# Optimization experiments

Measured on AMD Instinct MI355X. Metric: run time of the kernel, lower is better.

Reference implementation:

```python
import jax, jax.numpy as jnp
import numpy as np

NEG_SLOPE = 0.2  # PyG GATConv default


def gat_conv(h, src, dst, n_nodes, W, a_src, a_dst, bias, concat):
    """PyG-style GATConv (single linear shared across src/dst, self-loops
    already included in src/dst). W: [heads*out, in]; a_*: [heads, out]."""
    heads, out = a_src.shape
    g = (h @ W.T).reshape(-1, heads, out)  # [N, H, D]
    # per-node attention logits, then gather scalars per edge (PyG order)
    al_src = jnp.einsum('nhd,hd->nh', g, a_src)  # [N, H]
    al_dst = jnp.einsum('nhd,hd->nh', g, a_dst)
    e = jax.nn.leaky_relu(al_src[src] + al_dst[dst], NEG_SLOPE)  # [E, H]
    # segment softmax over incoming edges of each dst node
    e_max = jax.ops.segment_max(e, dst, num_segments=n_nodes)
    e_exp = jnp.exp(e - e_max[dst])
    denom = jax.ops.segment_sum(e_exp, dst, num_segments=n_nodes)
    alpha = e_exp / denom[dst]  # every node has a self-loop -> denom > 0
    msg = g[src] * alpha[..., None]  # [E, H, D]
    out_n = jax.ops.segment_sum(msg, dst, num_segments=n_nodes)  # [N, H, D]
    if concat:
        out_n = out_n.reshape(n_nodes, heads * out)
    else:
        out_n = out_n.mean(axis=1)
    return out_n + bias


def setup_inputs() -> dict:
    key = jax.random.key(0)
    ks = jax.random.split(key, 20)
    N, M = 100000, 1600000
    node_dim, edge_dim, global_dim = 12, 5, 11
    hidden, heads, num_targets = 32, 4, 4
    in1 = node_dim + global_dim  # 23
    s = 0.1
    inp = {
        'x': jax.random.normal(ks[0], (N, node_dim), jnp.float32),
        'edge_index': jax.random.randint(ks[1], (2, M), 0, N, jnp.int32),
        'edge_attr': jax.random.normal(ks[2], (M, edge_dim), jnp.float32),
        'u': jax.random.normal(ks[3], (1, global_dim), jnp.float32),
        # conv1: in1 -> hidden per head, concat
        'W1': jax.random.normal(ks[4], (heads * hidden, in1), jnp.float32) * s,
        'a_src1': jax.random.normal(ks[5], (heads, hidden), jnp.float32) * s,
        'a_dst1': jax.random.normal(ks[6], (heads, hidden), jnp.float32) * s,
        'b1': jnp.zeros((heads * hidden,), jnp.float32),
        # conv2: heads*hidden -> hidden, mean over heads
        'W2': jax.random.normal(ks[7], (heads * hidden, heads * hidden), jnp.float32) * s,
        'a_src2': jax.random.normal(ks[8], (heads, hidden), jnp.float32) * s,
        'a_dst2': jax.random.normal(ks[9], (heads, hidden), jnp.float32) * s,
        'b2': jnp.zeros((hidden,), jnp.float32),
        # decoder: (2*hidden + edge_dim) -> 2*hidden -> hidden -> num_targets
        'dw1': jax.random.normal(ks[10], (2 * hidden, 2 * hidden + edge_dim), jnp.float32) * s,
        'db1': jnp.zeros((2 * hidden,), jnp.float32),
        'dw2': jax.random.normal(ks[11], (hidden, 2 * hidden), jnp.float32) * s,
        'db2': jnp.zeros((hidden,), jnp.float32),
        'dw3': jax.random.normal(ks[12], (num_targets, hidden), jnp.float32) * s,
        'db3': jnp.zeros((num_targets,), jnp.float32),
    }
    return inp


def reference(x, edge_index, edge_attr, u, W1, a_src1, a_dst1, b1,
              W2, a_src2, a_dst2, b2, dw1, db1, dw2, db2, dw3, db3):
    N = x.shape[0]
    loop = jnp.arange(N, dtype=edge_index.dtype)
    src = jnp.concatenate([edge_index[0], loop])  # add self-loops (PyG default)
    dst = jnp.concatenate([edge_index[1], loop])

    u_node = jnp.broadcast_to(u, (N, u.shape[-1]))
    h = jnp.concatenate([x, u_node], axis=-1)  # [N, 23]

    h = jax.nn.elu(gat_conv(h, src, dst, N, W1, a_src1, a_dst1, b1, True))
    h = jax.nn.elu(gat_conv(h, src, dst, N, W2, a_src2, a_dst2, b2, False))

    s0, d0 = edge_index[0], edge_index[1]
    e_in = jnp.concatenate([h[s0], h[d0], edge_attr], axis=-1)  # [M, 69]
    z = jax.nn.relu(e_in @ dw1.T + db1)
    z = jax.nn.relu(z @ dw2.T + db2)
    return z @ dw3.T + db3  # [M, num_targets]
```

## Files before the change

### kernel.cpp

```cpp
#include <hip/hip_runtime.h>

#define DEVINL __device__ __forceinline__

DEVINL float leakyf(float v) { return v > 0.f ? v : 0.2f * v; }
DEVINL float eluf(float v)   { return v > 0.f ? v : __expf(v) - 1.f; }

__global__ void __launch_bounds__(256) k_izero(int* __restrict__ p, int total) {
  int t = blockIdx.x * blockDim.x + threadIdx.x;
  if (t < total) p[t] = 0;
}

__global__ void __launch_bounds__(256) k_count(const int* __restrict__ ei,
                                               int* __restrict__ cnt, int M, int E) {
  int e = blockIdx.x * blockDim.x + threadIdx.x;
  if (e >= E) return;
  int d = (e < M) ? ei[M + e] : e - M;
  atomicAdd(&cnt[d], 1);
}

__global__ void __launch_bounds__(256) k_scan1(const int* __restrict__ cnt,
                                               int* __restrict__ off,
                                               int* __restrict__ bsum, int N) {
  __shared__ int sh[256];
  int i = blockIdx.x * 256 + threadIdx.x;
  int v = (i < N) ? cnt[i] : 0;
  sh[threadIdx.x] = v;
  __syncthreads();
  for (int o = 1; o < 256; o <<= 1) {
    int t = (threadIdx.x >= o) ? sh[threadIdx.x - o] : 0;
    __syncthreads();
    sh[threadIdx.x] += t;
    __syncthreads();
  }
  if (i < N) off[i] = sh[threadIdx.x] - v;
  if (threadIdx.x == 255) bsum[blockIdx.x] = sh[255];
}

__global__ void __launch_bounds__(512) k_scan2(int* __restrict__ bsum, int nb) {
  __shared__ int sh[512];
  int t = threadIdx.x;
  int v = (t < nb) ? bsum[t] : 0;
  sh[t] = v;
  __syncthreads();
  for (int o = 1; o < 512; o <<= 1) {
    int x = (t >= o) ? sh[t - o] : 0;
    __syncthreads();
    sh[t] += x;
    __syncthreads();
  }
  if (t < nb) bsum[t] = sh[t] - v;
}

__global__ void __launch_bounds__(256) k_scan3(int* __restrict__ off,
                                               const int* __restrict__ bsum,
                                               int* __restrict__ cur, int N, int E) {
  int i = blockIdx.x * 256 + threadIdx.x;
  if (i < N) { off[i] += bsum[i >> 8]; cur[i] = 0; }
  if (i == N) off[N] = E;
}

__global__ void __launch_bounds__(256) k_fill(const int* __restrict__ ei,
                                              const int* __restrict__ off,
                                              int* __restrict__ cur,
                                              int* __restrict__ ssrc,
                                              int* __restrict__ idst,
                                              int* __restrict__ ieid, int M, int E) {
  int e = blockIdx.x * blockDim.x + threadIdx.x;
  if (e >= E) return;
  int s, d, id;
  if (e < M) { s = ei[e]; d = ei[M + e]; id = e; }
  else       { s = e - M; d = s; id = -1; }
  int pos = off[d] + atomicAdd(&cur[d], 1);
  ssrc[pos] = s;
  idst[pos] = d;
  ieid[pos] = id;
}

__global__ void k_prep(const float* __restrict__ W1, const float* __restrict__ as1,
                       const float* __restrict__ ad1,
                       const float* __restrict__ W2, const float* __restrict__ as2,
                       const float* __restrict__ ad2,
                       float* __restrict__ wa1s, float* __restrict__ wa1d,
                       float* __restrict__ wa2s, float* __restrict__ wa2d) {
  int t = threadIdx.x;
  if (t < 92) {
    int h = t / 23, c = t % 23;
    float s1 = 0.f, s2 = 0.f;
    for (int dd = 0; dd < 32; ++dd) {
      float w = W1[(h * 32 + dd) * 23 + c];
      s1 += w * as1[h * 32 + dd];
      s2 += w * ad1[h * 32 + dd];
    }
    wa1s[t] = s1;
    wa1d[t] = s2;
  }
  {
    int h = t >> 7, c = t & 127;
    float s1 = 0.f, s2 = 0.f;
    for (int dd = 0; dd < 32; ++dd) {
      float w = W2[(h * 32 + dd) * 128 + c];
      s1 += w * as2[h * 32 + dd];
      s2 += w * ad2[h * 32 + dd];
    }
    wa2s[t] = s1;
    wa2d[t] = s2;
  }
}

__global__ void __launch_bounds__(128) k_g1(
    const float* __restrict__ x, const float* __restrict__ u,
    const float* __restrict__ W1,
    const float* __restrict__ wa1s, const float* __restrict__ wa1d,
    float* __restrict__ g1, float* __restrict__ al1s, float* __restrict__ al1d) {
  int n = blockIdx.x, k = threadIdx.x;
  __shared__ float hs[23];
  if (k < 12) hs[k] = x[n * 12 + k];
  else if (k < 23) hs[k] = u[k - 12];
  __syncthreads();
  const float* w = W1 + k * 23;
  float s = 0.f;
#pragma unroll
  for (int c = 0; c < 23; ++c) s += hs[c] * w[c];
  g1[n * 128 + k] = s;
  if (k < 8) {
    int h = k & 3;
    const float* wa = (k < 4 ? wa1s : wa1d) + h * 23;
    float t = 0.f;
#pragma unroll
    for (int c = 0; c < 23; ++c) t += hs[c] * wa[c];
    (k < 4 ? al1s : al1d)[n * 4 + h] = t;
  }
}

template <int MODE>
__global__ void __launch_bounds__(128) k_gat(
    const float* __restrict__ g, const float* __restrict__ als,
    const float* __restrict__ ald, const int* __restrict__ off,
    const int* __restrict__ ssrc, const float* __restrict__ bias,
    float* __restrict__ outp) {
  int d = blockIdx.x, t = threadIdx.x, h = t >> 5;
  float av = ald[d * 4 + h];
  int p0 = off[d], p1 = off[d + 1];
  float acc = 0.f, den = 0.f;
  int p = p0;
  for (; p + 4 <= p1; p += 4) {
    int s0 = ssrc[p], s1 = ssrc[p + 1], s2 = ssrc[p + 2], s3 = ssrc[p + 3];
    float l0 = als[s0 * 4 + h], l1 = als[s1 * 4 + h];
    float l2 = als[s2 * 4 + h], l3 = als[s3 * 4 + h];
    float g0 = g[(size_t)s0 * 128 + t], g1v = g[(size_t)s1 * 128 + t];
    float g2v = g[(size_t)s2 * 128 + t], g3v = g[(size_t)s3 * 128 + t];
    float w0 = __expf(leakyf(l0 + av)), w1 = __expf(leakyf(l1 + av));
    float w2 = __expf(leakyf(l2 + av)), w3 = __expf(leakyf(l3 + av));
    acc += w0 * g0 + w1 * g1v + w2 * g2v + w3 * g3v;
    den += (w0 + w1) + (w2 + w3);
  }
  for (; p < p1; ++p) {
    int s = ssrc[p];
    float w = __expf(leakyf(als[s * 4 + h] + av));
    acc += w * g[(size_t)s * 128 + t];
    den += w;
  }
  float v = acc / den;
  if (MODE == 0) {
    outp[(size_t)d * 128 + t] = eluf(v + bias[t]);
  } else {
    __shared__ float sh[128];
    sh[t] = v;
    __syncthreads();
    if (t < 32) {
      float m = 0.25f * (sh[t] + sh[t + 32] + sh[t + 64] + sh[t + 96]);
      outp[(size_t)d * 32 + t] = eluf(m + bias[t]);
    }
  }
}

__global__ void __launch_bounds__(128) k_g2t(
    const float* __restrict__ h2, const float* __restrict__ W2,
    const float* __restrict__ wa2s, const float* __restrict__ wa2d,
    float* __restrict__ g2, float* __restrict__ al2s, float* __restrict__ al2d,
    int N, int ntiles) {
  __shared__ float4 w4s[128][32];
  __shared__ float4 hs4[32][32];
  int t = threadIdx.x;

  for (int i = t; i < 4096; i += 128) {
    int c = i >> 5, kk = i & 31;
    float4 v = *(const float4*)(W2 + c * 128 + kk * 4);
    w4s[c][kk ^ ((c >> 2) & 31)] = v;
  }

  int m = t & 31, grp = t >> 5;
  int c0 = 4 * m;

  for (int tile = blockIdx.x; tile < ntiles; tile += gridDim.x) {
    int n0 = tile * 32;
    __syncthreads();
    for (int i = t; i < 1024; i += 128) {
      int n = i >> 5, kk = i & 31;
      int nn = n0 + n;
      hs4[n][kk] = (nn < N) ? *(const float4*)(h2 + (size_t)nn * 128 + kk * 4)
                            : make_float4(0.f, 0.f, 0.f, 0.f);
    }
    __syncthreads();

    float acc[8][4];
#pragma unroll
    for (int n = 0; n < 8; ++n)
#pragma unroll
      for (int j = 0; j < 4; ++j) acc[n][j] = 0.f;

#pragma unroll 8
    for (int kk = 0; kk < 32; ++kk) {
      float4 wj[4];
#pragma unroll
      for (int j = 0; j < 4; ++j) wj[j] = w4s[c0 + j][kk ^ m];
#pragma unroll
      for (int n = 0; n < 8; ++n) {
        float4 hv = hs4[grp * 8 + n][kk];
#pragma unroll
        for (int j = 0; j < 4; ++j) {
          acc[n][j] += hv.x * wj[j].x + hv.y * wj[j].y +
                       hv.z * wj[j].z + hv.w * wj[j].w;
        }
      }
    }
#pragma unroll
    for (int n = 0; n < 8; ++n) {
      int nn = n0 + grp * 8 + n;
      if (nn < N)
        *(float4*)(g2 + (size_t)nn * 128 + c0) =
            make_float4(acc[n][0], acc[n][1], acc[n][2], acc[n][3]);
    }

    for (int v = 0; v < 2; ++v) {
      int idx = t + 128 * v;
      int n = idx >> 3, j = idx & 7, h = j & 3;
      int nn = n0 + n;
      if (nn < N) {
        const float4* wa = (const float4*)((j < 4 ? wa2s : wa2d) + h * 128);
        float s = 0.f;
#pragma unroll
        for (int kk = 0; kk < 32; ++kk) {
          float4 a = hs4[n][kk];
          float4 w = wa[kk];
          s += a.x * w.x + a.y * w.y + a.z * w.z + a.w * w.w;
        }
        (j < 4 ? al2s : al2d)[(size_t)nn * 4 + h] = s;
      }
    }
  }
}

__global__ void __launch_bounds__(256) k_pq(
    const float* __restrict__ h3, const float* __restrict__ dw1,
    float* __restrict__ pq, int N) {
  __shared__ float4 ws4[64][16];
  __shared__ float ht[64][32];
  int t = threadIdx.x;
  for (int i = t; i < 4096; i += 256) {
    int k = i >> 6, c = i & 63;
    ((float*)&ws4[k][(c >> 2) ^ (k & 15)])[c & 3] = dw1[k * 69 + c];
  }
  int n0 = blockIdx.x * 64;
  for (int i = t; i < 2048; i += 256) {
    int n = i >> 5, c = i & 31;
    int nn = n0 + n;
    ht[n][c] = (nn < N) ? h3[(size_t)nn * 32 + c] : 0.f;
  }
  __syncthreads();
  int k2 = t & 127, sub = t >> 7;
  int k = k2 & 63, base4 = (k2 < 64) ? 0 : 8;
  float4 wr[8];
#pragma unroll
  for (int i = 0; i < 8; ++i) wr[i] = ws4[k][(base4 + i) ^ (k & 15)];
  for (int ii = 0; ii < 32; ++ii) {
    int n = sub * 32 + ii;
    const float4* hr = (const float4*)ht[n];
    float s = 0.f;
#pragma unroll
    for (int i = 0; i < 8; ++i) {
      float4 a = hr[i], w = wr[i];
      s += a.x * w.x + a.y * w.y + a.z * w.z + a.w * w.w;
    }
    int nn = n0 + n;
    if (nn < N) pq[(size_t)nn * 128 + k2] = s;
  }
}

__global__ void __launch_bounds__(256) k_dec(
    const float* __restrict__ pq, const int* __restrict__ ssrc,
    const int* __restrict__ idst, const int* __restrict__ ieid,
    const float* __restrict__ ea,
    const float* __restrict__ dw1, const float* __restrict__ db1,
    const float* __restrict__ dw2, const float* __restrict__ db2,
    const float* __restrict__ dw3, const float* __restrict__ db3,
    float* __restrict__ out, int E) {
  __shared__ float cs[64][8];
  __shared__ float w2s[32 * 64];
  __shared__ float w3s[4 * 32];
  __shared__ float bbs[104];
  int t = threadIdx.x;
  for (int i = t; i < 512; i += 256) {
    int k = i >> 3, c = i & 7;
    cs[k][c] = (c < 5) ? dw1[k * 69 + 64 + c] : 0.f;
  }
  for (int i = t; i < 2048; i += 256) w2s[i] = dw2[i];
  if (t < 128) w3s[t] = dw3[t];
  if (t < 64) bbs[t] = db1[t];
  else if (t < 96) bbs[t] = db2[t - 64];
  else if (t < 100) bbs[t] = db3[t - 96];
  __syncthreads();

  int pos = blockIdx.x * 256 + t;
  if (pos >= E) return;
  int eid = ieid[pos];
  if (eid < 0) return;
  int s = ssrc[pos], d = idst[pos];
  const float4* Pp = (const float4*)(pq + (size_t)s * 128);
  const float4* Qp = (const float4*)(pq + (size_t)d * 128 + 64);
  const float* ep = ea + (size_t)eid * 5;
  float e0 = ep[0], e1 = ep[1], e2 = ep[2], e3 = ep[3], e4 = ep[4];

  float z1[64];
#pragma unroll
  for (int i = 0; i < 16; ++i) {
    float4 p = Pp[i], q = Qp[i];
    z1[4 * i + 0] = p.x + q.x;
    z1[4 * i + 1] = p.y + q.y;
    z1[4 * i + 2] = p.z + q.z;
    z1[4 * i + 3] = p.w + q.w;
  }
#pragma unroll
  for (int k = 0; k < 64; ++k) {
    float acc = z1[k] + bbs[k];
    acc += cs[k][0] * e0 + cs[k][1] * e1 + cs[k][2] * e2 + cs[k][3] * e3 +
           cs[k][4] * e4;
    z1[k] = fmaxf(acc, 0.f);
  }

  float z2[32];
#pragma unroll
  for (int k = 0; k < 32; ++k) z2[k] = bbs[64 + k];
#pragma unroll
  for (int cq = 0; cq < 16; ++cq) {
    float4 e = make_float4(z1[cq * 4], z1[cq * 4 + 1], z1[cq * 4 + 2],
                           z1[cq * 4 + 3]);
#pragma unroll
    for (int k = 0; k < 32; ++k) {
      float4 w = *(const float4*)(w2s + k * 64 + cq * 4);
      z2[k] += e.x * w.x + e.y * w.y + e.z * w.z + e.w * w.w;
    }
  }
#pragma unroll
  for (int k = 0; k < 32; ++k) z2[k] = fmaxf(z2[k], 0.f);

  float o0 = bbs[96], o1 = bbs[97], o2 = bbs[98], o3 = bbs[99];
#pragma unroll
  for (int cq = 0; cq < 8; ++cq) {
    float4 e = make_float4(z2[cq * 4], z2[cq * 4 + 1], z2[cq * 4 + 2],
                           z2[cq * 4 + 3]);
    float4 wa = *(const float4*)(w3s + 0 * 32 + cq * 4);
    float4 wb = *(const float4*)(w3s + 1 * 32 + cq * 4);
    float4 wc = *(const float4*)(w3s + 2 * 32 + cq * 4);
    float4 wd = *(const float4*)(w3s + 3 * 32 + cq * 4);
    o0 += e.x * wa.x + e.y * wa.y + e.z * wa.z + e.w * wa.w;
    o1 += e.x * wb.x + e.y * wb.y + e.z * wb.z + e.w * wb.w;
    o2 += e.x * wc.x + e.y * wc.y + e.z * wc.z + e.w * wc.w;
    o3 += e.x * wd.x + e.y * wd.y + e.z * wd.z + e.w * wd.w;
  }
  *(float4*)(out + (size_t)eid * 4) = make_float4(o0, o1, o2, o3);
}

extern "C" void kernel_launch(void* const* d_in, const int* in_sizes, int n_in,
                              void* d_out, int out_size, void* d_ws, size_t ws_size,
                              hipStream_t stream) {
  const float* x   = (const float*)d_in[0];
  const int*   ei  = (const int*)d_in[1];
  const float* ea  = (const float*)d_in[2];
  const float* u   = (const float*)d_in[3];
  const float* W1  = (const float*)d_in[4];
  const float* as1 = (const float*)d_in[5];
  const float* ad1 = (const float*)d_in[6];
  const float* b1  = (const float*)d_in[7];
  const float* W2  = (const float*)d_in[8];
  const float* as2 = (const float*)d_in[9];
  const float* ad2 = (const float*)d_in[10];
  const float* b2  = (const float*)d_in[11];
  const float* dw1 = (const float*)d_in[12];
  const float* db1 = (const float*)d_in[13];
  const float* dw2 = (const float*)d_in[14];
  const float* db2 = (const float*)d_in[15];
  const float* dw3 = (const float*)d_in[16];
  const float* db3 = (const float*)d_in[17];
  float* out = (float*)d_out;

  const int N = in_sizes[0] / 12;
  const int M = in_sizes[1] / 2;
  const int E = M + N;

  float* ws = (float*)d_ws;
  float* A    = ws;
  float* B    = A + (size_t)N * 128;
  float* H3   = B;
  float* AL1S = B + (size_t)N * 128;
  float* AL1D = AL1S + (size_t)N * 4;
  float* AL2S = AL1D + (size_t)N * 4;
  float* AL2D = AL2S + (size_t)N * 4;
  float* WA1S = AL2D + (size_t)N * 4;
  float* WA1D = WA1S + 96;
  float* WA2S = WA1D + 96;
  float* WA2D = WA2S + 512;
  int* IOFF = (int*)(WA2D + 512);
  int* ICUR = IOFF + (N + 1);
  int* IBS  = ICUR + N;
  int* ISRC = IBS + 512;
  int* IDST = ISRC + E;
  int* IEID = IDST + E;

  int nb = (N + 255) / 256;
  int gE = (E + 255) / 256;

  k_izero<<<nb, 256, 0, stream>>>(ICUR, N);
  k_count<<<gE, 256, 0, stream>>>(ei, ICUR, M, E);
  k_scan1<<<nb, 256, 0, stream>>>(ICUR, IOFF, IBS, N);
  k_scan2<<<1, 512, 0, stream>>>(IBS, nb);
  k_scan3<<<(N + 256) / 256, 256, 0, stream>>>(IOFF, IBS, ICUR, N, E);
  k_fill<<<gE, 256, 0, stream>>>(ei, IOFF, ICUR, ISRC, IDST, IEID, M, E);

  k_prep<<<1, 512, 0, stream>>>(W1, as1, ad1, W2, as2, ad2, WA1S, WA1D, WA2S, WA2D);

  k_g1<<<N, 128, 0, stream>>>(x, u, W1, WA1S, WA1D, A, AL1S, AL1D);
  k_gat<0><<<N, 128, 0, stream>>>(A, AL1S, AL1D, IOFF, ISRC, b1, B);

  int ntiles = (N + 31) / 32;
  k_g2t<<<512, 128, 0, stream>>>(B, W2, WA2S, WA2D, A, AL2S, AL2D, N, ntiles);
  k_gat<1><<<N, 128, 0, stream>>>(A, AL2S, AL2D, IOFF, ISRC, b2, H3);

  k_pq<<<(N + 63) / 64, 256, 0, stream>>>(H3, dw1, A, N);
  k_dec<<<gE, 256, 0, stream>>>(A, ISRC, IDST, IEID, ea, dw1, db1, dw2, db2,
                                dw3, db3, out, E);
}
```

Baseline: 1.122 ms.

## Map one wavefront per node in GAT and process two edges per thread in decoder

The GAT aggregation kernels now assign one 64-lane wavefront per destination node. Each lane handles two features through float2 loads, and four nodes share each 256-thread block. The head-mean reduction uses shuffles in place of shared memory and a block barrier. The edge decoder now has each thread process two edges, so every weight read from LDS is reused across both edges, and the weights are stored as float4. This targets per-block overhead, LDS traffic and barriers, at the cost of higher register pressure in the decoder (two 32-float accumulators plus the inputs).

```diff
diff --git a/kernel.cpp b/kernel.cpp
--- a/kernel.cpp
+++ b/kernel.cpp
@@ -133,43 +133,59 @@
 }
 
 template <int MODE>
-__global__ void __launch_bounds__(128) k_gat(
+__global__ void __launch_bounds__(256) k_gat(
     const float* __restrict__ g, const float* __restrict__ als,
     const float* __restrict__ ald, const int* __restrict__ off,
     const int* __restrict__ ssrc, const float* __restrict__ bias,
-    float* __restrict__ outp) {
-  int d = blockIdx.x, t = threadIdx.x, h = t >> 5;
+    float* __restrict__ outp, int N) {
+  int wid = threadIdx.x >> 6, lane = threadIdx.x & 63;
+  int d = blockIdx.x * 4 + wid;
+  if (d >= N) return;
+  int h = lane >> 4;
   float av = ald[d * 4 + h];
   int p0 = off[d], p1 = off[d + 1];
-  float acc = 0.f, den = 0.f;
+  float accx = 0.f, accy = 0.f, den = 0.f;
   int p = p0;
   for (; p + 4 <= p1; p += 4) {
     int s0 = ssrc[p], s1 = ssrc[p + 1], s2 = ssrc[p + 2], s3 = ssrc[p + 3];
     float l0 = als[s0 * 4 + h], l1 = als[s1 * 4 + h];
     float l2 = als[s2 * 4 + h], l3 = als[s3 * 4 + h];
-    float g0 = g[(size_t)s0 * 128 + t], g1v = g[(size_t)s1 * 128 + t];
-    float g2v = g[(size_t)s2 * 128 + t], g3v = g[(size_t)s3 * 128 + t];
+    float2 G0 = *(const float2*)(g + (size_t)s0 * 128 + 2 * lane);
+    float2 G1 = *(const float2*)(g + (size_t)s1 * 128 + 2 * lane);
+    float2 G2 = *(const float2*)(g + (size_t)s2 * 128 + 2 * lane);
+    float2 G3 = *(const float2*)(g + (size_t)s3 * 128 + 2 * lane);
     float w0 = __expf(leakyf(l0 + av)), w1 = __expf(leakyf(l1 + av));
     float w2 = __expf(leakyf(l2 + av)), w3 = __expf(leakyf(l3 + av));
-    acc += w0 * g0 + w1 * g1v + w2 * g2v + w3 * g3v;
+    accx += w0 * G0.x + w1 * G1.x + w2 * G2.x + w3 * G3.x;
+    accy += w0 * G0.y + w1 * G1.y + w2 * G2.y + w3 * G3.y;
     den += (w0 + w1) + (w2 + w3);
   }
   for (; p < p1; ++p) {
     int s = ssrc[p];
     float w = __expf(leakyf(als[s * 4 + h] + av));
-    acc += w * g[(size_t)s * 128 + t];
+    float2 G = *(const float2*)(g + (size_t)s * 128 + 2 * lane);
+    accx += w * G.x;
+    accy += w * G.y;
     den += w;
   }
-  float v = acc / den;
+  float inv = 1.f / den;
+  float vx = accx * inv, vy = accy * inv;
   if (MODE == 0) {
-    outp[(size_t)d * 128 + t] = eluf(v + bias[t]);
+    float2 b = *(const float2*)(bias + 2 * lane);
+    float2 o;
+    o.x = eluf(vx + b.x);
+    o.y = eluf(vy + b.y);
+    *(float2*)(outp + (size_t)d * 128 + 2 * lane) = o;
   } else {
-    __shared__ float sh[128];
-    sh[t] = v;
-    __syncthreads();
-    if (t < 32) {
-      float m = 0.25f * (sh[t] + sh[t + 32] + sh[t + 64] + sh[t + 96]);
-      outp[(size_t)d * 32 + t] = eluf(m + bias[t]);
+    float sx = vx + __shfl_xor(vx, 16);
+    sx += __shfl_xor(sx, 32);
+    float sy = vy + __shfl_xor(vy, 16);
+    sy += __shfl_xor(sy, 32);
+    if (lane < 16) {
+      float2 o;
+      o.x = eluf(0.25f * sx + bias[2 * lane]);
+      o.y = eluf(0.25f * sy + bias[2 * lane + 1]);
+      *(float2*)(outp + (size_t)d * 32 + 2 * lane) = o;
     }
   }
 }
@@ -295,80 +311,120 @@
     const float* __restrict__ dw2, const float* __restrict__ db2,
     const float* __restrict__ dw3, const float* __restrict__ db3,
     float* __restrict__ out, int E) {
-  __shared__ float cs[64][8];
-  __shared__ float w2s[32 * 64];
-  __shared__ float w3s[4 * 32];
-  __shared__ float bbs[104];
+  __shared__ float4 w2s4[32][16];
+  __shared__ float4 ct4[5][16];
+  __shared__ float4 b1q[16];
+  __shared__ float4 b2q[8];
+  __shared__ float4 w3s4[4][8];
+  __shared__ float  db3s[4];
   int t = threadIdx.x;
   for (int i = t; i < 512; i += 256) {
-    int k = i >> 3, c = i & 7;
-    cs[k][c] = (c < 5) ? dw1[k * 69 + 64 + c] : 0.f;
-  }
-  for (int i = t; i < 2048; i += 256) w2s[i] = dw2[i];
-  if (t < 128) w3s[t] = dw3[t];
-  if (t < 64) bbs[t] = db1[t];
-  else if (t < 96) bbs[t] = db2[t - 64];
-  else if (t < 100) bbs[t] = db3[t - 96];
+    int k = i >> 4, cq = i & 15;
+    w2s4[k][cq] = *(const float4*)(dw2 + k * 64 + cq * 4);
+  }
+  if (t < 80) {
+    int c = t / 16, cq = t % 16;
+    float4 v;
+    v.x = dw1[(4 * cq + 0) * 69 + 64 + c];
+    v.y = dw1[(4 * cq + 1) * 69 + 64 + c];
+    v.z = dw1[(4 * cq + 2) * 69 + 64 + c];
+    v.w = dw1[(4 * cq + 3) * 69 + 64 + c];
+    ct4[c][cq] = v;
+  } else if (t < 96) {
+    b1q[t - 80] = *(const float4*)(db1 + 4 * (t - 80));
+  } else if (t < 104) {
+    b2q[t - 96] = *(const float4*)(db2 + 4 * (t - 96));
+  } else if (t < 136) {
+    int o = (t - 104) >> 3, cq = (t - 104) & 7;
+    w3s4[o][cq] = *(const float4*)(dw3 + o * 32 + 4 * cq);
+  } else if (t < 140) {
+    db3s[t - 136] = db3[t - 136];
+  }
   __syncthreads();
 
-  int pos = blockIdx.x * 256 + t;
-  if (pos >= E) return;
-  int eid = ieid[pos];
-  if (eid < 0) return;
-  int s = ssrc[pos], d = idst[pos];
-  const float4* Pp = (const float4*)(pq + (size_t)s * 128);
-  const float4* Qp = (const float4*)(pq + (size_t)d * 128 + 64);
-  const float* ep = ea + (size_t)eid * 5;
-  float e0 = ep[0], e1 = ep[1], e2 = ep[2], e3 = ep[3], e4 = ep[4];
-
-  float z1[64];
-#pragma unroll
-  for (int i = 0; i < 16; ++i) {
-    float4 p = Pp[i], q = Qp[i];
-    z1[4 * i + 0] = p.x + q.x;
-    z1[4 * i + 1] = p.y + q.y;
-    z1[4 * i + 2] = p.z + q.z;
-    z1[4 * i + 3] = p.w + q.w;
-  }
-#pragma unroll
-  for (int k = 0; k < 64; ++k) {
-    float acc = z1[k] + bbs[k];
-    acc += cs[k][0] * e0 + cs[k][1] * e1 + cs[k][2] * e2 + cs[k][3] * e3 +
-           cs[k][4] * e4;
-    z1[k] = fmaxf(acc, 0.f);
-  }
-
-  float z2[32];
-#pragma unroll
-  for (int k = 0; k < 32; ++k) z2[k] = bbs[64 + k];
-#pragma unroll
+  int pos0 = blockIdx.x * 512 + t;
+  int pos1 = pos0 + 256;
+  bool okA = pos0 < E, okB = pos1 < E;
+  int pa = okA ? pos0 : 0, pb = okB ? pos1 : 0;
+  int eA_ = okA ? ieid[pa] : -1;
+  int eB_ = okB ? ieid[pb] : -1;
+  bool wA = eA_ >= 0, wB = eB_ >= 0;
+  int eidA = wA ? eA_ : 0, eidB = wB ? eB_ : 0;
+  int sA = ssrc[pa], dA = idst[pa];
+  int sB = ssrc[pb], dB = idst[pb];
+  const float4* PA = (const float4*)(pq + (size_t)sA * 128);
+  const float4* QA = (const float4*)(pq + (size_t)dA * 128 + 64);
+  const float4* PB = (const float4*)(pq + (size_t)sB * 128);
+  const float4* QB = (const float4*)(pq + (size_t)dB * 128 + 64);
+  const float* eap = ea + (size_t)eidA * 5;
+  const float* ebp = ea + (size_t)eidB * 5;
+  float eAv[5], eBv[5];
+#pragma unroll
+  for (int c = 0; c < 5; ++c) { eAv[c] = eap[c]; eBv[c] = ebp[c]; }
+
+  float z2a[32], z2b[32];
+#pragma unroll
+  for (int kq = 0; kq < 8; ++kq) {
+    float4 b = b2q[kq];
+    z2a[4 * kq + 0] = b.x; z2a[4 * kq + 1] = b.y;
+    z2a[4 * kq + 2] = b.z; z2a[4 * kq + 3] = b.w;
+    z2b[4 * kq + 0] = b.x; z2b[4 * kq + 1] = b.y;
+    z2b[4 * kq + 2] = b.z; z2b[4 * kq + 3] = b.w;
+  }
+
   for (int cq = 0; cq < 16; ++cq) {
-    float4 e = make_float4(z1[cq * 4], z1[cq * 4 + 1], z1[cq * 4 + 2],
-                           z1[cq * 4 + 3]);
+    float4 pA = PA[cq], qA = QA[cq];
+    float4 pB = PB[cq], qB = QB[cq];
+    float4 bq = b1q[cq];
+    float4 zA, zB;
+    zA.x = pA.x + qA.x + bq.x; zA.y = pA.y + qA.y + bq.y;
+    zA.z = pA.z + qA.z + bq.z; zA.w = pA.w + qA.w + bq.w;
+    zB.x = pB.x + qB.x + bq.x; zB.y = pB.y + qB.y + bq.y;
+    zB.z = pB.z + qB.z + bq.z; zB.w = pB.w + qB.w + bq.w;
+#pragma unroll
+    for (int c = 0; c < 5; ++c) {
+      float4 cc = ct4[c][cq];
+      float ca = eAv[c], cb = eBv[c];
+      zA.x += ca * cc.x; zA.y += ca * cc.y; zA.z += ca * cc.z; zA.w += ca * cc.w;
+      zB.x += cb * cc.x; zB.y += cb * cc.y; zB.z += cb * cc.z; zB.w += cb * cc.w;
+    }
+    zA.x = fmaxf(zA.x, 0.f); zA.y = fmaxf(zA.y, 0.f);
+    zA.z = fmaxf(zA.z, 0.f); zA.w = fmaxf(zA.w, 0.f);
+    zB.x = fmaxf(zB.x, 0.f); zB.y = fmaxf(zB.y, 0.f);
+    zB.z = fmaxf(zB.z, 0.f); zB.w = fmaxf(zB.w, 0.f);
 #pragma unroll
     for (int k = 0; k < 32; ++k) {
-      float4 w = *(const float4*)(w2s + k * 64 + cq * 4);
-      z2[k] += e.x * w.x + e.y * w.y + e.z * w.z + e.w * w.w;
-    }
-  }
-#pragma unroll
-  for (int k = 0; k < 32; ++k) z2[k] = fmaxf(z2[k], 0.f);
-
-  float o0 = bbs[96], o1 = bbs[97], o2 = bbs[98], o3 = bbs[99];
+      float4 w = w2s4[k][cq];
+      z2a[k] += w.x * zA.x + w.y * zA.y + w.z * zA.z + w.w * zA.w;
+      z2b[k] += w.x * zB.x + w.y * zB.y + w.z * zB.z + w.w * zB.w;
+    }
+  }
+#pragma unroll
+  for (int k = 0; k < 32; ++k) {
+    z2a[k] = fmaxf(z2a[k], 0.f);
+    z2b[k] = fmaxf(z2b[k], 0.f);
+  }
+
+  float oA[4], oB[4];
+#pragma unroll
+  for (int o = 0; o < 4; ++o) { oA[o] = db3s[o]; oB[o] = db3s[o]; }
 #pragma unroll
   for (int cq = 0; cq < 8; ++cq) {
-    float4 e = make_float4(z2[cq * 4], z2[cq * 4 + 1], z2[cq * 4 + 2],
-                           z2[cq * 4 + 3]);
-    float4 wa = *(const float4*)(w3s + 0 * 32 + cq * 4);
-    float4 wb = *(const float4*)(w3s + 1 * 32 + cq * 4);
-    float4 wc = *(const float4*)(w3s + 2 * 32 + cq * 4);
-    float4 wd = *(const float4*)(w3s + 3 * 32 + cq * 4);
-    o0 += e.x * wa.x + e.y * wa.y + e.z * wa.z + e.w * wa.w;
-    o1 += e.x * wb.x + e.y * wb.y + e.z * wb.z + e.w * wb.w;
-    o2 += e.x * wc.x + e.y * wc.y + e.z * wc.z + e.w * wc.w;
-    o3 += e.x * wd.x + e.y * wd.y + e.z * wd.z + e.w * wd.w;
-  }
-  *(float4*)(out + (size_t)eid * 4) = make_float4(o0, o1, o2, o3);
+    float ax = z2a[4 * cq], ay = z2a[4 * cq + 1];
+    float az = z2a[4 * cq + 2], aw = z2a[4 * cq + 3];
+    float bx = z2b[4 * cq], by = z2b[4 * cq + 1];
+    float bz = z2b[4 * cq + 2], bw = z2b[4 * cq + 3];
+#pragma unroll
+    for (int o = 0; o < 4; ++o) {
+      float4 w = w3s4[o][cq];
+      oA[o] += ax * w.x + ay * w.y + az * w.z + aw * w.w;
+      oB[o] += bx * w.x + by * w.y + bz * w.z + bw * w.w;
+    }
+  }
+  if (wA && okA)
+    *(float4*)(out + (size_t)eidA * 4) = make_float4(oA[0], oA[1], oA[2], oA[3]);
+  if (wB && okB)
+    *(float4*)(out + (size_t)eidB * 4) = make_float4(oB[0], oB[1], oB[2], oB[3]);
 }
 
 extern "C" void kernel_launch(void* const* d_in, const int* in_sizes, int n_in,
@@ -430,13 +486,13 @@
   k_prep<<<1, 512, 0, stream>>>(W1, as1, ad1, W2, as2, ad2, WA1S, WA1D, WA2S, WA2D);
 
   k_g1<<<N, 128, 0, stream>>>(x, u, W1, WA1S, WA1D, A, AL1S, AL1D);
-  k_gat<0><<<N, 128, 0, stream>>>(A, AL1S, AL1D, IOFF, ISRC, b1, B);
+  k_gat<0><<<(N + 3) / 4, 256, 0, stream>>>(A, AL1S, AL1D, IOFF, ISRC, b1, B, N);
 
   int ntiles = (N + 31) / 32;
   k_g2t<<<512, 128, 0, stream>>>(B, W2, WA2S, WA2D, A, AL2S, AL2D, N, ntiles);
-  k_gat<1><<<N, 128, 0, stream>>>(A, AL2S, AL2D, IOFF, ISRC, b2, H3);
+  k_gat<1><<<(N + 3) / 4, 256, 0, stream>>>(A, AL2S, AL2D, IOFF, ISRC, b2, H3, N);
 
   k_pq<<<(N + 63) / 64, 256, 0, stream>>>(H3, dw1, A, N);
-  k_dec<<<gE, 256, 0, stream>>>(A, ISRC, IDST, IEID, ea, dw1, db1, dw2, db2,
-                                dw3, db3, out, E);
-}
+  k_dec<<<(E + 511) / 512, 256, 0, stream>>>(A, ISRC, IDST, IEID, ea, dw1, db1,
+                                             dw2, db2, dw3, db3, out, E);
+}
```

Measured after the change: 1.080 ms. 1.04x faster.
